# Kernel optimization log

Measured on AMD Instinct MI355X. Metric: run time of the kernel, lower is better.

## Reference

```python
import jax, jax.numpy as jnp
import numpy as np

N_ENTITIES = 100000
N_USERS = 100000
N_ITEMS = 50000
N_ASPECTS = 64
CHANNEL = 64
N_EDGES = 1250000
N_RELATIONS = 16


def setup_inputs() -> dict:
    key = jax.random.key(0)
    ks = jax.random.split(key, 9)
    entity_emb = jax.random.normal(ks[0], (N_ENTITIES, CHANNEL), dtype=jnp.float32)
    item_emb = jax.random.normal(ks[1], (N_ITEMS, CHANNEL), dtype=jnp.float32)
    user_emb = jax.random.normal(ks[2], (N_USERS, CHANNEL), dtype=jnp.float32)
    aspect_emb = jax.random.normal(ks[3], (N_ASPECTS, CHANNEL), dtype=jnp.float32)
    edge_index = jax.random.randint(ks[4], (2, N_EDGES), 0, N_ENTITIES, dtype=jnp.int64)
    # edge_type values in [2, N_RELATIONS+2) since forward does weight[edge_type - 2]
    edge_type = jax.random.randint(ks[5], (N_EDGES,), 0, N_RELATIONS, dtype=jnp.int64) + 2
    # dense stand-ins for the sparse interaction matrices (n_aspects is small)
    ua_interact_mat = jax.random.uniform(ks[6], (N_USERS, N_ASPECTS), dtype=jnp.float32)
    ia_interact_mat = jax.random.uniform(ks[7], (N_ITEMS, N_ASPECTS), dtype=jnp.float32)
    weight = jax.random.normal(ks[8], (N_RELATIONS, CHANNEL), dtype=jnp.float32)
    return {
        "entity_emb": entity_emb, "item_emb": item_emb, "user_emb": user_emb,
        "aspect_emb": aspect_emb, "edge_index": edge_index, "edge_type": edge_type,
        "ua_interact_mat": ua_interact_mat, "ia_interact_mat": ia_interact_mat,
        "weight": weight,
    }


def reference(entity_emb, item_emb, user_emb, aspect_emb, edge_index, edge_type,
              ua_interact_mat, ia_interact_mat, weight):
    n_entities = entity_emb.shape[0]
    head, tail = edge_index[0], edge_index[1]

    # KG aggregate: gather tail entity + relation embeddings, multiply, scatter-mean by head
    edge_relation_emb = weight[edge_type - 2]          # [E, C]
    neigh_relation_emb = entity_emb[tail] * edge_relation_emb  # [E, C]
    sums = jax.ops.segment_sum(neigh_relation_emb, head, num_segments=n_entities)
    counts = jax.ops.segment_sum(jnp.ones(head.shape, dtype=neigh_relation_emb.dtype),
                                 head, num_segments=n_entities)
    entity_agg = sums / jnp.clip(counts, 1.0)[:, None]  # scatter_mean (0 where empty)

    # user->aspect attention (softmax over aspects; sum over aspect dim)
    score_ua = jax.nn.softmax(user_emb @ aspect_emb.T, axis=1)   # [U, A]
    score_ia = jax.nn.softmax(item_emb @ aspect_emb.T, axis=1)   # [I, A]

    user_agg = ua_interact_mat @ aspect_emb                      # [U, C]
    user_agg = user_agg * score_ua.sum(axis=1, keepdims=True) + user_agg

    item_agg = ia_interact_mat @ aspect_emb                      # [I, C]
    item_agg = item_agg * score_ia.sum(axis=1, keepdims=True) + item_agg

    return (item_agg, entity_agg, user_agg)
```

## Files before the change

### kernel.cpp

```cpp
#include <hip/hip_runtime.h>

#define N_EDGES   1250000
#define N_ENT     100000
#define N_USR     100000
#define N_ITM     50000
#define CH        64
#define CAP       48

#define ITEM_TILES ((N_ITM + 63) / 64)
#define USER_TILES ((N_USR + 63) / 64)
#define TOT_TILES  (ITEM_TILES + USER_TILES)

#define EPT 2
#define SCAT_BLKS ((N_EDGES + 256*EPT - 1) / (256*EPT))

__device__ __forceinline__ unsigned short bf16_rne(float f) {
    unsigned u = __float_as_uint(f);
    unsigned r = u + 0x7FFFu + ((u >> 16) & 1u);
    return (unsigned short)(r >> 16);
}

__global__ __launch_bounds__(256, 4) void scatter_gemm_kernel(
    const int*   __restrict__ edge_index,
    const int*   __restrict__ edge_type,
    const float* __restrict__ entity_emb,
    const float* __restrict__ aspect_emb,
    const float* __restrict__ ia_mat,
    const float* __restrict__ ua_mat,
    unsigned* __restrict__ cursor,
    unsigned* __restrict__ keys,
    unsigned short* __restrict__ ent16,
    float* __restrict__ out_item,
    float* __restrict__ out_user)
{
    {
        const int eA = blockIdx.x * (256 * EPT) + threadIdx.x;
        const int eB = eA + 256;
        const bool vA = (eA < N_EDGES);
        const bool vB = (eB < N_EDGES);
        const int la = vA ? eA : 0;
        const int lb = vB ? eB : 0;

        int headA = __builtin_nontemporal_load(&edge_index[la]);
        int headB = __builtin_nontemporal_load(&edge_index[lb]);
        int tailA = __builtin_nontemporal_load(&edge_index[N_EDGES + la]);
        int tailB = __builtin_nontemporal_load(&edge_index[N_EDGES + lb]);
        int relA  = __builtin_nontemporal_load(&edge_type[la]) - 2;
        int relB  = __builtin_nontemporal_load(&edge_type[lb]) - 2;

        unsigned posA = 0xFFFFFFFFu, posB = 0xFFFFFFFFu;
        if (vA) posA = atomicAdd(&cursor[headA], 1u);
        if (vB) posB = atomicAdd(&cursor[headB], 1u);

        if (vA && posA < CAP)
            keys[(unsigned)headA * CAP + posA] =
                (unsigned)tailA | ((unsigned)relA << 20);
        if (vB && posB < CAP)
            keys[(unsigned)headB * CAP + posB] =
                (unsigned)tailB | ((unsigned)relB << 20);
    }

    if (ent16) {
        const int tid = blockIdx.x * 256 + threadIdx.x;
        const int nth = SCAT_BLKS * 256;
        const float4* src = (const float4*)entity_emb;
        ushort4* dst = (ushort4*)ent16;
        for (int g = tid; g < N_ENT * 16; g += nth) {
            float4 v = src[g];
            ushort4 o;
            o.x = bf16_rne(v.x); o.y = bf16_rne(v.y);
            o.z = bf16_rne(v.z); o.w = bf16_rne(v.w);
            dst[g] = o;
        }
    }

    int tile = blockIdx.x;
    if (tile >= TOT_TILES) return;

    const float* M; float* out; int N, tt;
    if (tile < ITEM_TILES) { M = ia_mat; out = out_item; N = N_ITM; tt = tile; }
    else                   { M = ua_mat; out = out_user; N = N_USR; tt = tile - ITEM_TILES; }
    const int row0 = tt * 64;

    const int t  = threadIdx.x;
    const int ci = t & 15;
    const int r0 = (t >> 4) * 4;

    const float4* A4 = (const float4*)aspect_emb;
    const float4* M4 = (const float4*)M;

    int r[4];
    #pragma unroll
    for (int j = 0; j < 4; ++j) {
        int rr = row0 + r0 + j;
        r[j] = (rr < N) ? rr : (N - 1);
    }

    float4 acc[4];
    #pragma unroll
    for (int j = 0; j < 4; ++j) acc[j] = make_float4(0.f, 0.f, 0.f, 0.f);

    #pragma unroll 4
    for (int k4 = 0; k4 < 16; ++k4) {
        float4 a0 = A4[(k4 * 4 + 0) * 16 + ci];
        float4 a1 = A4[(k4 * 4 + 1) * 16 + ci];
        float4 a2 = A4[(k4 * 4 + 2) * 16 + ci];
        float4 a3 = A4[(k4 * 4 + 3) * 16 + ci];
        #pragma unroll
        for (int j = 0; j < 4; ++j) {
            float4 mv = M4[(size_t)r[j] * 16 + k4];
            acc[j].x += mv.x * a0.x + mv.y * a1.x + mv.z * a2.x + mv.w * a3.x;
            acc[j].y += mv.x * a0.y + mv.y * a1.y + mv.z * a2.y + mv.w * a3.y;
            acc[j].z += mv.x * a0.z + mv.y * a1.z + mv.z * a2.z + mv.w * a3.z;
            acc[j].w += mv.x * a0.w + mv.y * a1.w + mv.z * a2.w + mv.w * a3.w;
        }
    }

    float4* out4 = (float4*)out;
    #pragma unroll
    for (int j = 0; j < 4; ++j) {
        int rr = row0 + r0 + j;
        if (rr < N) {
            float4 v = acc[j];
            v.x *= 2.f; v.y *= 2.f; v.z *= 2.f; v.w *= 2.f;
            out4[(size_t)rr * 16 + ci] = v;
        }
    }
}

__global__ __launch_bounds__(256, 4) void reduce_bf16_kernel(
    const unsigned short* __restrict__ ent16,
    const float* __restrict__ weight,
    const unsigned* __restrict__ cursor,
    const unsigned* __restrict__ keys,
    float* __restrict__ out_ent)
{
    const int gtid = blockIdx.x * 256 + threadIdx.x;
    const int wave = gtid >> 6;
    const int lane = threadIdx.x & 63;
    const int half = lane >> 5;
    const int l32  = lane & 31;
    const int slot = l32 >> 3;
    const int q    = lane & 7;

    const int ent = wave * 2 + half;

    unsigned c = cursor[ent];
    if (c > CAP) c = CAP;
    const unsigned* bucket = keys + (unsigned)ent * CAP;

    const int nk = ((int)c > slot) ? (int)((c - (unsigned)slot + 3u) >> 2) : 0;

    unsigned kr[12];
    #pragma unroll
    for (int i = 0; i < 12; ++i)
        kr[i] = (i < nk) ? __builtin_nontemporal_load(&bucket[slot + 4 * i]) : 0u;

    const uint4*  e16 = (const uint4*)ent16;
    const float4* w4  = (const float4*)weight;

    float4 acc0 = make_float4(0.f, 0.f, 0.f, 0.f);
    float4 acc1 = make_float4(0.f, 0.f, 0.f, 0.f);

    #pragma unroll
    for (int i = 0; i < 12; ++i) {
        if (i < nk) {
            unsigned key  = kr[i];
            unsigned tail = key & 0xFFFFFu;
            unsigned rel  = key >> 20;
            uint4 ev = e16[(size_t)tail * 8 + q];
            const float4* wp = w4 + rel * 16 + q * 2;
            float4 w0 = wp[0], w1 = wp[1];
            float e0 = __uint_as_float(ev.x << 16);
            float e1 = __uint_as_float(ev.x & 0xFFFF0000u);
            float e2 = __uint_as_float(ev.y << 16);
            float e3 = __uint_as_float(ev.y & 0xFFFF0000u);
            float e4 = __uint_as_float(ev.z << 16);
            float e5 = __uint_as_float(ev.z & 0xFFFF0000u);
            float e6 = __uint_as_float(ev.w << 16);
            float e7 = __uint_as_float(ev.w & 0xFFFF0000u);
            acc0.x += e0 * w0.x; acc0.y += e1 * w0.y;
            acc0.z += e2 * w0.z; acc0.w += e3 * w0.w;
            acc1.x += e4 * w1.x; acc1.y += e5 * w1.y;
            acc1.z += e6 * w1.z; acc1.w += e7 * w1.w;
        }
    }

    #pragma unroll
    for (int off = 8; off <= 16; off <<= 1) {
        acc0.x += __shfl_xor(acc0.x, off); acc0.y += __shfl_xor(acc0.y, off);
        acc0.z += __shfl_xor(acc0.z, off); acc0.w += __shfl_xor(acc0.w, off);
        acc1.x += __shfl_xor(acc1.x, off); acc1.y += __shfl_xor(acc1.y, off);
        acc1.z += __shfl_xor(acc1.z, off); acc1.w += __shfl_xor(acc1.w, off);
    }

    if (slot == 0) {
        float inv = 1.0f / fmaxf((float)c, 1.0f);
        acc0.x *= inv; acc0.y *= inv; acc0.z *= inv; acc0.w *= inv;
        acc1.x *= inv; acc1.y *= inv; acc1.z *= inv; acc1.w *= inv;
        float4* o = (float4*)out_ent + (size_t)ent * 16 + q * 2;
        o[0] = acc0;
        o[1] = acc1;
    }
}

__global__ __launch_bounds__(256, 4) void reduce_kernel(
    const float* __restrict__ entity_emb,
    const float* __restrict__ weight,
    const unsigned* __restrict__ cursor,
    const unsigned* __restrict__ keys,
    float* __restrict__ out_ent)
{
    const int gtid = blockIdx.x * 256 + threadIdx.x;
    const int wave = gtid >> 6;
    const int lane = threadIdx.x & 63;
    const int half = lane >> 5;
    const int l32  = lane & 31;
    const int slot = l32 >> 3;
    const int q    = lane & 7;

    const int ent = wave * 2 + half;

    unsigned c = cursor[ent];
    if (c > CAP) c = CAP;
    const unsigned* bucket = keys + (unsigned)ent * CAP;

    const int nk = ((int)c > slot) ? (int)((c - (unsigned)slot + 3u) >> 2) : 0;

    unsigned kr[12];
    #pragma unroll
    for (int i = 0; i < 12; ++i)
        kr[i] = (i < nk) ? __builtin_nontemporal_load(&bucket[slot + 4 * i]) : 0u;

    const float4* emb4 = (const float4*)entity_emb;
    const float4* w4   = (const float4*)weight;

    float4 acc0 = make_float4(0.f, 0.f, 0.f, 0.f);
    float4 acc1 = make_float4(0.f, 0.f, 0.f, 0.f);

    #pragma unroll
    for (int i = 0; i < 12; ++i) {
        if (i < nk) {
            unsigned key  = kr[i];
            unsigned tail = key & 0xFFFFFu;
            unsigned rel  = key >> 20;
            const float4* ep = emb4 + (size_t)tail * 16 + q * 2;
            const float4* wp = w4 + rel * 16 + q * 2;
            float4 e0 = ep[0], e1 = ep[1];
            float4 w0 = wp[0], w1 = wp[1];
            acc0.x += e0.x * w0.x; acc0.y += e0.y * w0.y;
            acc0.z += e0.z * w0.z; acc0.w += e0.w * w0.w;
            acc1.x += e1.x * w1.x; acc1.y += e1.y * w1.y;
            acc1.z += e1.z * w1.z; acc1.w += e1.w * w1.w;
        }
    }

    #pragma unroll
    for (int off = 8; off <= 16; off <<= 1) {
        acc0.x += __shfl_xor(acc0.x, off); acc0.y += __shfl_xor(acc0.y, off);
        acc0.z += __shfl_xor(acc0.z, off); acc0.w += __shfl_xor(acc0.w, off);
        acc1.x += __shfl_xor(acc1.x, off); acc1.y += __shfl_xor(acc1.y, off);
        acc1.z += __shfl_xor(acc1.z, off); acc1.w += __shfl_xor(acc1.w, off);
    }

    if (slot == 0) {
        float inv = 1.0f / fmaxf((float)c, 1.0f);
        acc0.x *= inv; acc0.y *= inv; acc0.z *= inv; acc0.w *= inv;
        acc1.x *= inv; acc1.y *= inv; acc1.z *= inv; acc1.w *= inv;
        float4* o = (float4*)out_ent + (size_t)ent * 16 + q * 2;
        o[0] = acc0;
        o[1] = acc1;
    }
}

__global__ __launch_bounds__(256) void scatter_kernel(
    const float* __restrict__ entity_emb,
    const int* __restrict__ edge_index, const int* __restrict__ edge_type,
    const float* __restrict__ weight,
    float* __restrict__ ent_sum, float* __restrict__ cnt)
{
    int idx = blockIdx.x * 256 + threadIdx.x;
    int e = idx >> 4;
    int q = idx & 15;
    if (e >= N_EDGES) return;
    int head = edge_index[e];
    int tail = edge_index[N_EDGES + e];
    int rel  = edge_type[e] - 2;
    const float4* emb4 = (const float4*)entity_emb;
    const float4* w4   = (const float4*)weight;
    float4 ev = emb4[(size_t)tail * 16 + q];
    float4 wv = w4[rel * 16 + q];
    float* dst = ent_sum + (size_t)head * 64 + q * 4;
    atomicAdd(dst + 0, ev.x * wv.x);
    atomicAdd(dst + 1, ev.y * wv.y);
    atomicAdd(dst + 2, ev.z * wv.z);
    atomicAdd(dst + 3, ev.w * wv.w);
    if (q == 0) atomicAdd(&cnt[head], 1.0f);
}

__global__ __launch_bounds__(256) void divide_kernel(
    float* __restrict__ ent, const float* __restrict__ cnt)
{
    int idx = blockIdx.x * 256 + threadIdx.x;
    if (idx >= N_ENT * 16) return;
    int row = idx >> 4;
    float inv = 1.0f / fmaxf(cnt[row], 1.0f);
    float4* p = (float4*)ent;
    float4 v = p[idx];
    v.x *= inv; v.y *= inv; v.z *= inv; v.w *= inv;
    p[idx] = v;
}

__global__ __launch_bounds__(256) void gemm_fallback_kernel(
    const float* __restrict__ ia, const float* __restrict__ ua,
    const float* __restrict__ A,
    float* __restrict__ out_item, float* __restrict__ out_user)
{
    int tile = blockIdx.x;
    const float* M; float* out; int N, tt;
    if (tile < ITEM_TILES) { M = ia; out = out_item; N = N_ITM; tt = tile; }
    else                   { M = ua; out = out_user; N = N_USR; tt = tile - ITEM_TILES; }
    const int row0 = tt * 64;
    const int t  = threadIdx.x;
    const int ci = t & 15;
    const int r0 = (t >> 4) * 4;
    const float4* A4 = (const float4*)A;
    const float4* M4 = (const float4*)M;
    int r[4];
    #pragma unroll
    for (int j = 0; j < 4; ++j) {
        int rr = row0 + r0 + j;
        r[j] = (rr < N) ? rr : (N - 1);
    }
    float4 acc[4];
    #pragma unroll
    for (int j = 0; j < 4; ++j) acc[j] = make_float4(0.f, 0.f, 0.f, 0.f);
    #pragma unroll 4
    for (int k4 = 0; k4 < 16; ++k4) {
        float4 a0 = A4[(k4 * 4 + 0) * 16 + ci];
        float4 a1 = A4[(k4 * 4 + 1) * 16 + ci];
        float4 a2 = A4[(k4 * 4 + 2) * 16 + ci];
        float4 a3 = A4[(k4 * 4 + 3) * 16 + ci];
        #pragma unroll
        for (int j = 0; j < 4; ++j) {
            float4 mv = M4[(size_t)r[j] * 16 + k4];
            acc[j].x += mv.x * a0.x + mv.y * a1.x + mv.z * a2.x + mv.w * a3.x;
            acc[j].y += mv.x * a0.y + mv.y * a1.y + mv.z * a2.y + mv.w * a3.y;
            acc[j].z += mv.x * a0.z + mv.y * a1.z + mv.z * a2.z + mv.w * a3.z;
            acc[j].w += mv.x * a0.w + mv.y * a1.w + mv.z * a2.w + mv.w * a3.w;
        }
    }
    float4* out4 = (float4*)out;
    #pragma unroll
    for (int j = 0; j < 4; ++j) {
        int rr = row0 + r0 + j;
        if (rr < N) {
            float4 v = acc[j];
            v.x *= 2.f; v.y *= 2.f; v.z *= 2.f; v.w *= 2.f;
            out4[(size_t)rr * 16 + ci] = v;
        }
    }
}

extern "C" void kernel_launch(void* const* d_in, const int* in_sizes, int n_in,
                              void* d_out, int out_size, void* d_ws, size_t ws_size,
                              hipStream_t stream) {
    const float* entity_emb = (const float*)d_in[0];
    const float* aspect_emb = (const float*)d_in[3];
    const int*   edge_index = (const int*)d_in[4];
    const int*   edge_type  = (const int*)d_in[5];
    const float* ua_mat     = (const float*)d_in[6];
    const float* ia_mat     = (const float*)d_in[7];
    const float* weight     = (const float*)d_in[8];

    float* out_item = (float*)d_out;
    float* out_ent  = out_item + (size_t)N_ITM * CH;
    float* out_user = out_ent  + (size_t)N_ENT * CH;

    size_t need_fc = ((size_t)N_ENT + (size_t)N_ENT * CAP) * 4;
    size_t need_bf = need_fc + (size_t)N_ENT * CH * 2;

    if (ws_size >= need_fc) {
        unsigned* cursor = (unsigned*)d_ws;
        unsigned* keys   = cursor + N_ENT;
        unsigned short* ent16 = (ws_size >= need_bf)
            ? (unsigned short*)(keys + (size_t)N_ENT * CAP) : nullptr;

        (void)hipMemsetAsync(cursor, 0, (size_t)N_ENT * 4, stream);
        scatter_gemm_kernel<<<SCAT_BLKS, 256, 0, stream>>>(
            edge_index, edge_type, entity_emb, aspect_emb, ia_mat, ua_mat,
            cursor, keys, ent16, out_item, out_user);
        if (ent16) {
            reduce_bf16_kernel<<<(N_ENT / 2) * 64 / 256, 256, 0, stream>>>(
                ent16, weight, cursor, keys, out_ent);
        } else {
            reduce_kernel<<<(N_ENT / 2) * 64 / 256, 256, 0, stream>>>(
                entity_emb, weight, cursor, keys, out_ent);
        }
    } else {
        float* cnt = (float*)d_ws;
        (void)hipMemsetAsync(out_ent, 0, (size_t)N_ENT * CH * sizeof(float), stream);
        (void)hipMemsetAsync(cnt, 0, (size_t)N_ENT * sizeof(float), stream);
        scatter_kernel<<<(N_EDGES * 16 + 255) / 256, 256, 0, stream>>>(
            entity_emb, edge_index, edge_type, weight, out_ent, cnt);
        divide_kernel<<<(N_ENT * 16 + 255) / 256, 256, 0, stream>>>(out_ent, cnt);
        gemm_fallback_kernel<<<TOT_TILES, 256, 0, stream>>>(
            ia_mat, ua_mat, aspect_emb, out_item, out_user);
    }
}
```

Baseline: 299.4 us.

## Give each entity a full wave in reduce and hoist bf16 conversion loads

The reduce kernel now assigns one 64-lane wave per entity instead of half a wave. It uses 8 key slots with a 6-deep unrolled key list, and adds one more shuffle-reduction stage. Occupancy hints rise to 8 blocks per SM. In the scatter kernel, the float-to-bf16 entity conversion loads are issued up front, before the edge atomics, in a fixed 3-iteration unrolled form so their latency overlaps the scatter. This doubles the reduce launch size and its shuffle work, and the fixed 3-iteration conversion assumes the grid covers all entity rows.

```diff
diff --git a/kernel.cpp b/kernel.cpp
--- a/kernel.cpp
+++ b/kernel.cpp
@@ -33,6 +33,21 @@
     float* __restrict__ out_item,
     float* __restrict__ out_user)
 {
+    const int tid = blockIdx.x * 256 + threadIdx.x;
+    const int nth = SCAT_BLKS * 256;
+
+    bool  cvalid[3];
+    float4 cv[3];
+    {
+        const float4* src = (const float4*)entity_emb;
+        #pragma unroll
+        for (int k = 0; k < 3; ++k) {
+            int g = tid + k * nth;
+            cvalid[k] = (ent16 != nullptr) && (g < N_ENT * 16);
+            cv[k] = cvalid[k] ? src[g] : make_float4(0.f, 0.f, 0.f, 0.f);
+        }
+    }
+
     {
         const int eA = blockIdx.x * (256 * EPT) + threadIdx.x;
         const int eB = eA + 256;
@@ -60,17 +75,17 @@
                 (unsigned)tailB | ((unsigned)relB << 20);
     }
 
-    if (ent16) {
-        const int tid = blockIdx.x * 256 + threadIdx.x;
-        const int nth = SCAT_BLKS * 256;
-        const float4* src = (const float4*)entity_emb;
+    {
         ushort4* dst = (ushort4*)ent16;
-        for (int g = tid; g < N_ENT * 16; g += nth) {
-            float4 v = src[g];
-            ushort4 o;
-            o.x = bf16_rne(v.x); o.y = bf16_rne(v.y);
-            o.z = bf16_rne(v.z); o.w = bf16_rne(v.w);
-            dst[g] = o;
+        #pragma unroll
+        for (int k = 0; k < 3; ++k) {
+            if (cvalid[k]) {
+                int g = tid + k * nth;
+                ushort4 o;
+                o.x = bf16_rne(cv[k].x); o.y = bf16_rne(cv[k].y);
+                o.z = bf16_rne(cv[k].z); o.w = bf16_rne(cv[k].w);
+                dst[g] = o;
+            }
         }
     }
 
@@ -128,7 +143,7 @@
     }
 }
 
-__global__ __launch_bounds__(256, 4) void reduce_bf16_kernel(
+__global__ __launch_bounds__(256, 8) void reduce_bf16_kernel(
     const unsigned short* __restrict__ ent16,
     const float* __restrict__ weight,
     const unsigned* __restrict__ cursor,
@@ -136,25 +151,21 @@
     float* __restrict__ out_ent)
 {
     const int gtid = blockIdx.x * 256 + threadIdx.x;
-    const int wave = gtid >> 6;
+    const int ent  = gtid >> 6;
     const int lane = threadIdx.x & 63;
-    const int half = lane >> 5;
-    const int l32  = lane & 31;
-    const int slot = l32 >> 3;
+    const int slot = lane >> 3;
     const int q    = lane & 7;
-
-    const int ent = wave * 2 + half;
 
     unsigned c = cursor[ent];
     if (c > CAP) c = CAP;
     const unsigned* bucket = keys + (unsigned)ent * CAP;
 
-    const int nk = ((int)c > slot) ? (int)((c - (unsigned)slot + 3u) >> 2) : 0;
-
-    unsigned kr[12];
-    #pragma unroll
-    for (int i = 0; i < 12; ++i)
-        kr[i] = (i < nk) ? __builtin_nontemporal_load(&bucket[slot + 4 * i]) : 0u;
+    const int nk = ((int)c > slot) ? (int)((c - (unsigned)slot + 7u) >> 3) : 0;
+
+    unsigned kr[6];
+    #pragma unroll
+    for (int i = 0; i < 6; ++i)
+        kr[i] = (i < nk) ? __builtin_nontemporal_load(&bucket[slot + 8 * i]) : 0u;
 
     const uint4*  e16 = (const uint4*)ent16;
     const float4* w4  = (const float4*)weight;
@@ -163,7 +174,7 @@
     float4 acc1 = make_float4(0.f, 0.f, 0.f, 0.f);
 
     #pragma unroll
-    for (int i = 0; i < 12; ++i) {
+    for (int i = 0; i < 6; ++i) {
         if (i < nk) {
             unsigned key  = kr[i];
             unsigned tail = key & 0xFFFFFu;
@@ -187,7 +198,7 @@
     }
 
     #pragma unroll
-    for (int off = 8; off <= 16; off <<= 1) {
+    for (int off = 8; off <= 32; off <<= 1) {
         acc0.x += __shfl_xor(acc0.x, off); acc0.y += __shfl_xor(acc0.y, off);
         acc0.z += __shfl_xor(acc0.z, off); acc0.w += __shfl_xor(acc0.w, off);
         acc1.x += __shfl_xor(acc1.x, off); acc1.y += __shfl_xor(acc1.y, off);
@@ -391,7 +402,7 @@
             edge_index, edge_type, entity_emb, aspect_emb, ia_mat, ua_mat,
             cursor, keys, ent16, out_item, out_user);
         if (ent16) {
-            reduce_bf16_kernel<<<(N_ENT / 2) * 64 / 256, 256, 0, stream>>>(
+            reduce_bf16_kernel<<<(N_ENT * 64) / 256, 256, 0, stream>>>(
                 ent16, weight, cursor, keys, out_ent);
         } else {
             reduce_kernel<<<(N_ENT / 2) * 64 / 256, 256, 0, stream>>>(
```

Measured after the change: 291.9 us. 1.03x faster.
